# Kernel optimization log

Measured on AMD Instinct MI355X. Metric: run time of the kernel, lower is better.

Reference implementation:

```python
import jax, jax.numpy as jnp
import numpy as np

B = 64        # graphs per batch
N = 2048      # nodes per graph
BN = B * N
BE = BN * 16  # edges (avg degree 16)
C1 = 64
C2 = 64
M = 16
K_EDGES = 4   # hardcoded k=4 in original forward


def setup_inputs() -> dict:
    key = jax.random.key(0)
    k1, k2, k3, k4, k5, k6 = jax.random.split(key, 6)
    x = jax.random.normal(k1, (BN, C1), dtype=jnp.float32)
    e_ = jax.random.randint(k2, (2, BE), 0, BN, dtype=jnp.int32)
    b_ = jnp.repeat(jnp.arange(B, dtype=jnp.int32), N)  # sorted batch index
    # Linear params (stored as (in, out); torch stores (out, in))
    W_assign = jax.random.normal(k3, (C1, M), dtype=jnp.float32) / np.sqrt(C1)
    b_assign = jax.random.normal(k4, (M,), dtype=jnp.float32) * 0.01
    W_embed = jax.random.normal(k5, (C1, C2 - 3), dtype=jnp.float32) / np.sqrt(C1)
    b_embed = jax.random.normal(k6, (C2 - 3,), dtype=jnp.float32) * 0.01
    return {"x": x, "e_": e_, "b_": b_, "W_assign": W_assign,
            "b_assign": b_assign, "W_embed": W_embed, "b_embed": b_embed}


def reference(x, e_, b_, W_assign, b_assign, W_embed, b_embed):
    BN_, _ = x.shape
    Bn = int(jnp.max(b_)) + 1
    Mm = W_assign.shape[1]

    p = x[:, :3]                                   # (BN, 3) positions
    f = x @ W_embed + b_embed                      # (BN, C2-3)
    S = jax.nn.softmax(x @ W_assign + b_assign, axis=-1)  # (BN, M)

    # Weighted scatter-reduce pooling: index_add over (batch*M + m)
    # == per-batch segment_sum of S[n,m] * feat[n,c]
    Zf = jax.ops.segment_sum(S[:, :, None] * f[:, None, :], b_, num_segments=Bn)  # (B, M, C2-3)
    Zp = jax.ops.segment_sum(S[:, :, None] * p[:, None, :], b_, num_segments=Bn)  # (B, M, 3)
    w = jax.ops.segment_sum(S, b_, num_segments=Bn)                               # (B, M)
    w = jnp.maximum(w, 1e-10)
    Zp = Zp / w[..., None]
    x_out = jnp.concatenate([Zp, Zf], axis=-1).reshape(Bn * Mm, -1)  # (B*M, C2)

    # Sparse adjacency pooling: AS = A_NN @ S (A_NN[src,dst]=1 per edge)
    AS = jax.ops.segment_sum(S[e_[1]], e_[0], num_segments=BN_)  # (BN, M)
    # A_MM[b] = (S^T masked to batch b) @ AS
    A_MM = jax.ops.segment_sum(S[:, :, None] * AS[:, None, :], b_, num_segments=Bn)  # (B, M, M)

    # top-k edge construction on pooled adjacency
    dst = jax.lax.top_k(A_MM, K_EDGES)[1]                                # (B, M, k)
    src = jnp.broadcast_to(jnp.arange(Mm)[None, :, None], (Bn, Mm, K_EDGES))
    offset = (jnp.arange(Bn) * Mm)[:, None, None]
    e_out = jnp.stack([(src + offset).reshape(-1), (dst + offset).reshape(-1)], axis=0)
    b_out = jnp.repeat(jnp.arange(Bn), Mm)
    return x_out, e_out, b_out
```

## Files before the change

### kernel.cpp

```cpp
#include <hip/hip_runtime.h>

#define BN 131072
#define BE 2097152
#define NGR 64
#define CAP 36864

#define XS_OFF     0
#define WACC_OFF   262144
#define A_OFF      266240
#define ZERO_U4    20736
#define CUR_OFF    331776
#define QS_OFF     332032
#define ENDS_OFF   333056
#define SH_OFF     2430208
#define PK_OFF     6624512

__device__ __forceinline__ float bflo(unsigned u) { return __uint_as_float(u << 16); }
__device__ __forceinline__ float bfhi(unsigned u) { return __uint_as_float(u & 0xFFFF0000u); }

__global__ __launch_bounds__(256) void k_zero(uint4* __restrict__ zbase,
                                              int* __restrict__ cur)
{
    int zi = blockIdx.x * 256 + threadIdx.x;
    if (zi < ZERO_U4) zbase[zi] = make_uint4(0u, 0u, 0u, 0u);
    if (blockIdx.x == 0 && threadIdx.x < NGR) cur[threadIdx.x] = threadIdx.x * CAP;
}

__global__ __launch_bounds__(256) void k_scatter(const int* __restrict__ e_,
                                                 int* __restrict__ cur,
                                                 unsigned* __restrict__ packed)
{
    __shared__ int h[64];
    __shared__ int gb[64];
    int t = threadIdx.x;
    if (t < 64) h[t] = 0;
    __syncthreads();
    size_t base = (size_t)blockIdx.x * 4096;
    int e0v[16], e1v[16], rk[16];
    #pragma unroll
    for (int k = 0; k < 16; ++k) {
        size_t i = base + k * 256 + t;
        e0v[k] = e_[i];
        e1v[k] = e_[BE + i];
        rk[k] = atomicAdd(&h[e0v[k] >> 11], 1);
    }
    __syncthreads();
    if (t < 64) gb[t] = atomicAdd(&cur[t], h[t]);
    __syncthreads();
    #pragma unroll
    for (int k = 0; k < 16; ++k) {
        int b = e0v[k] >> 11;
        packed[gb[b] + rk[k]] = ((unsigned)(e0v[k] & 2047) << 17) | (unsigned)e1v[k];
    }
}

__global__ __launch_bounds__(256) void k_node(const float* __restrict__ x,
                                              const float* __restrict__ Wa,
                                              const float* __restrict__ ba,
                                              unsigned short* __restrict__ Sh,
                                              float* __restrict__ Xs,
                                              float* __restrict__ wacc)
{
    __shared__ __align__(16) float Xl[128 * 65];
    __shared__ __align__(16) float Sl[128 * 20];
    __shared__ float Wl[64 * 16];

    const int t = threadIdx.x;
    const int blk = blockIdx.x;
    const int g = blk >> 4;
    const int nd = t & 127;
    const int ch = t >> 7;

    const float4* xg4 = (const float4*)(x + (size_t)blk * 128 * 64);
    #pragma unroll
    for (int it = 0; it < 8; ++it) {
        int idx4 = it * 256 + t;
        float4 v = xg4[idx4];
        int node = idx4 >> 4;
        int c4 = (idx4 & 15) * 4;
        float* p = &Xl[node * 65 + c4];
        p[0] = v.x; p[1] = v.y; p[2] = v.z; p[3] = v.w;
    }
    for (int i = t; i < 1024; i += 256) Wl[i] = Wa[i];
    __syncthreads();

    float lg[16];
    #pragma unroll
    for (int m = 0; m < 16; ++m) lg[m] = 0.f;
    const int c0 = ch * 32;
    for (int c = c0; c < c0 + 32; ++c) {
        float xc = Xl[nd * 65 + c];
        #pragma unroll
        for (int m = 0; m < 16; ++m) lg[m] += xc * Wl[c * 16 + m];
    }
    float* Pl = Sl;
    if (ch == 1) {
        #pragma unroll
        for (int m = 0; m < 16; ++m) Pl[nd * 17 + m] = lg[m];
    }
    __syncthreads();

    float s[16];
    if (ch == 0) {
        float sum = 0.f, mx;
        #pragma unroll
        for (int m = 0; m < 16; ++m) lg[m] += ba[m] + Pl[nd * 17 + m];
        mx = lg[0];
        #pragma unroll
        for (int m = 1; m < 16; ++m) mx = fmaxf(mx, lg[m]);
        #pragma unroll
        for (int m = 0; m < 16; ++m) { s[m] = expf(lg[m] - mx); sum += s[m]; }
        float inv = 1.f / sum;
        #pragma unroll
        for (int m = 0; m < 16; ++m) s[m] *= inv;

        unsigned pk8[8];
        #pragma unroll
        for (int j = 0; j < 8; ++j) {
            unsigned b0 = __float_as_uint(s[2*j]);
            unsigned b1 = __float_as_uint(s[2*j+1]);
            unsigned h0 = (b0 + 0x7FFFu + ((b0 >> 16) & 1u)) >> 16;
            unsigned h1 = (b1 + 0x7FFFu + ((b1 >> 16) & 1u)) >> 16;
            pk8[j] = h0 | (h1 << 16);
        }
        uint4* hrow = (uint4*)(Sh + ((size_t)blk * 128 + nd) * 16);
        hrow[0] = make_uint4(pk8[0], pk8[1], pk8[2], pk8[3]);
        hrow[1] = make_uint4(pk8[4], pk8[5], pk8[6], pk8[7]);
    }
    __syncthreads();
    if (ch == 0) {
        #pragma unroll
        for (int q = 0; q < 4; ++q)
            *(float4*)(&Sl[nd * 20 + q * 4]) = make_float4(s[q*4], s[q*4+1], s[q*4+2], s[q*4+3]);
    }
    __syncthreads();

    const int c = t & 63;
    const int mg = t >> 6;
    float a0 = 0.f, a1 = 0.f, a2 = 0.f, a3 = 0.f;
    for (int n = 0; n < 128; ++n) {
        float xv = Xl[n * 65 + c];
        float4 sa = *(const float4*)(&Sl[n * 20 + mg * 4]);
        a0 += sa.x * xv; a1 += sa.y * xv; a2 += sa.z * xv; a3 += sa.w * xv;
    }
    float* xsg = Xs + g * 1024 + (mg * 4) * 64 + c;
    atomicAdd(&xsg[0],   a0);
    atomicAdd(&xsg[64],  a1);
    atomicAdd(&xsg[128], a2);
    atomicAdd(&xsg[192], a3);

    if (t < 16) {
        float ws_ = 0.f;
        for (int n = 0; n < 128; ++n) ws_ += Sl[n * 20 + t];
        atomicAdd(&wacc[g * 16 + t], ws_);
    }
}

#define SBUF_CAP 9216
__global__ __launch_bounds__(512) void k_sortL(unsigned* __restrict__ packed,
                                               const int* __restrict__ cur,
                                               int* __restrict__ qs,
                                               int* __restrict__ ends4)
{
    __shared__ unsigned sbuf[SBUF_CAP];
    __shared__ unsigned sout[SBUF_CAP];
    __shared__ int h[2048];
    __shared__ int psum[512];
    const int t = threadIdx.x;
    const int Q = blockIdx.x;
    const int g = Q >> 2;
    const int q = Q & 3;
    const int slab = g * CAP;
    const int n = cur[g] - slab;
    const int chunk = (n + 3) >> 2;
    const int qlo = slab + min(q * chunk, n);
    const int qhi = slab + min((q + 1) * chunk, n);
    const int nq = qhi - qlo;
    if (t == 0) qs[Q] = qlo;

    for (int i = t; i < 2048; i += 512) h[i] = 0;
    __syncthreads();
    for (int i = t; i < nq; i += 512) {
        unsigned u = packed[qlo + i];
        sbuf[i] = u;
        atomicAdd(&h[u >> 17], 1);
    }
    __syncthreads();

    int hl[4]; int s = 0;
    #pragma unroll
    for (int j = 0; j < 4; ++j) { hl[j] = h[t * 4 + j]; s += hl[j]; }
    psum[t] = s;
    __syncthreads();
    for (int off = 1; off < 512; off <<= 1) {
        int v = (t >= off) ? psum[t - off] : 0;
        __syncthreads();
        psum[t] += v;
        __syncthreads();
    }
    int run = psum[t] - s;
    int* ends = ends4 + (Q << 11);
    #pragma unroll
    for (int j = 0; j < 4; ++j) {
        int bin = t * 4 + j;
        int c = hl[j];
        h[bin] = run;
        run += c;
        ends[bin] = qlo + run;
    }
    __syncthreads();
    for (int i = t; i < nq; i += 512) {
        unsigned u = sbuf[i];
        int pos = atomicAdd(&h[u >> 17], 1);
        sout[pos] = u & 131071u;
    }
    __syncthreads();
    for (int i = t; i < nq; i += 512) packed[qlo + i] = sout[i];
}

__global__ __launch_bounds__(256) void k_edge(const unsigned* __restrict__ se1,
                                              const unsigned short* __restrict__ Sh,
                                              const int* __restrict__ ends4,
                                              const int* __restrict__ qs,
                                              float* __restrict__ A)
{
    __shared__ __align__(16) float ASl[64 * 16];
    const int t = threadIdx.x;
    const int blk = blockIdx.x;
    const int g = blk >> 5;
    const int nbase = blk << 6;

    {
        const int qd = t >> 2;
        const int c4 = (t & 3) << 2;
        const int nl = (nbase & 2047) + qd;
        const unsigned short* __restrict__ ShB = Sh + c4;

        int lo[4], hi[4];
        #pragma unroll
        for (int q = 0; q < 4; ++q) {
            const int Qb = (g << 2) + q;
            const int* __restrict__ ends = ends4 + (Qb << 11);
            lo[q] = nl ? ends[nl - 1] : qs[Qb];
            hi[q] = ends[nl];
        }

        float a0 = 0.f, a1 = 0.f, a2 = 0.f, a3 = 0.f;
        #pragma unroll
        for (int q = 0; q < 4; ++q) {
            int i = lo[q];
            const int h2 = hi[q];
            for (; i + 4 <= h2; i += 4) {
                unsigned ea = se1[i];
                unsigned eb = se1[i + 1];
                unsigned ec = se1[i + 2];
                unsigned ed = se1[i + 3];
                uint2 ra = *(const uint2*)(ShB + ((size_t)ea << 4));
                uint2 rb = *(const uint2*)(ShB + ((size_t)eb << 4));
                uint2 rc = *(const uint2*)(ShB + ((size_t)ec << 4));
                uint2 rd = *(const uint2*)(ShB + ((size_t)ed << 4));
                a0 += bflo(ra.x) + bflo(rb.x) + bflo(rc.x) + bflo(rd.x);
                a1 += bfhi(ra.x) + bfhi(rb.x) + bfhi(rc.x) + bfhi(rd.x);
                a2 += bflo(ra.y) + bflo(rb.y) + bflo(rc.y) + bflo(rd.y);
                a3 += bfhi(ra.y) + bfhi(rb.y) + bfhi(rc.y) + bfhi(rd.y);
            }
            for (; i < h2; ++i) {
                unsigned ea = se1[i];
                uint2 ra = *(const uint2*)(ShB + ((size_t)ea << 4));
                a0 += bflo(ra.x); a1 += bfhi(ra.x); a2 += bflo(ra.y); a3 += bfhi(ra.y);
            }
        }
        *(float4*)(&ASl[qd * 16 + c4]) = make_float4(a0, a1, a2, a3);
    }
    __syncthreads();

    {
        const int m = t >> 4;
        const int k = t & 15;
        const unsigned short* __restrict__ SgM = Sh + ((size_t)nbase << 4) + m;
        float a = 0.f;
        #pragma unroll 4
        for (int i = 0; i < 64; ++i) {
            float sv = __uint_as_float((unsigned)SgM[(size_t)i << 4] << 16);
            a += sv * ASl[i * 16 + k];
        }
        atomicAdd(&A[(g << 8) + t], a);
    }
}

__global__ __launch_bounds__(256) void k_xt(const float* __restrict__ Xs,
                                            const float* __restrict__ wacc,
                                            const float* __restrict__ We,
                                            const float* __restrict__ be,
                                            const float* __restrict__ A,
                                            float* __restrict__ out)
{
    const int t = threadIdx.x;
    const int blk = blockIdx.x;
    if (blk < 256) {
        int lane = t & 63;
        int row = blk * 4 + (t >> 6);
        const float* xs = Xs + row * 64;
        float w = wacc[row];
        float val;
        if (lane < 3) {
            val = xs[lane] / fmaxf(w, 1e-10f);
        } else {
            int c2 = lane - 3;
            float accv = w * be[c2];
            for (int cc = 0; cc < 64; ++cc) accv += xs[cc] * We[cc * 61 + c2];
            val = accv;
        }
        out[row * 64 + lane] = val;
    } else {
        int r = (blk - 256) * 256 + t;
        float v[16];
        #pragma unroll
        for (int i = 0; i < 16; ++i) v[i] = A[r * 16 + i];
        float* e0o = out + 65536;
        float* e1o = out + 65536 + 4096;
        float* bo  = out + 65536 + 8192;
        unsigned mask = 0;
        #pragma unroll
        for (int rep = 0; rep < 4; ++rep) {
            float best = -3.4e38f; int bi = 0;
            #pragma unroll
            for (int i = 0; i < 16; ++i) {
                bool ok = (((mask >> i) & 1u) == 0u) && (v[i] > best);
                if (ok) { best = v[i]; bi = i; }
            }
            mask |= (1u << bi);
            e0o[r * 4 + rep] = (float)r;
            e1o[r * 4 + rep] = (float)((r & ~15) + bi);
        }
        bo[r] = (float)(r >> 4);
    }
}

extern "C" void kernel_launch(void* const* d_in, const int* in_sizes, int n_in,
                              void* d_out, int out_size, void* d_ws, size_t ws_size,
                              hipStream_t stream)
{
    const float* x  = (const float*)d_in[0];
    const int*   e  = (const int*)d_in[1];
    const float* Wa = (const float*)d_in[3];
    const float* ba = (const float*)d_in[4];
    const float* We = (const float*)d_in[5];
    const float* be = (const float*)d_in[6];

    char* ws = (char*)d_ws;
    float* Xs     = (float*)(ws + XS_OFF);
    float* wacc   = (float*)(ws + WACC_OFF);
    float* A      = (float*)(ws + A_OFF);
    int*   cur    = (int*)(ws + CUR_OFF);
    int*   qs     = (int*)(ws + QS_OFF);
    int*   ends4  = (int*)(ws + ENDS_OFF);
    unsigned short* Sh = (unsigned short*)(ws + SH_OFF);
    unsigned* packed = (unsigned*)(ws + PK_OFF);

    k_zero    <<<82, 256, 0, stream>>>((uint4*)ws, cur);
    k_scatter <<<512, 256, 0, stream>>>(e, cur, packed);
    k_node    <<<1024, 256, 0, stream>>>(x, Wa, ba, Sh, Xs, wacc);
    k_sortL   <<<256, 512, 0, stream>>>(packed, cur, qs, ends4);
    k_edge    <<<2048, 256, 0, stream>>>(packed, Sh, ends4, qs, A);
    k_xt      <<<260, 256, 0, stream>>>(Xs, wacc, We, be, A, (float*)d_out);
}
```

Measured before the change: 93.77 us.

## Fuse node projection and per-graph edge sort into one launch

Merges the softmax/pooling node kernel and the local edge sort into a single heterogeneous launch. The first 256 blocks do the sort and the rest do node work, so the two independent stages overlap and one launch is dropped. The sort now uses 256 threads, re-reads packed from global instead of buffering it in shared memory, and shares a union shared buffer with the node path. That union raises per-block LDS for the node path. Also switches expf to __expf and stages W_embed in shared memory in the final kernel, which every block now loads, including the top-k blocks.

```diff
diff --git a/kernel.cpp b/kernel.cpp
--- a/kernel.cpp
+++ b/kernel.cpp
@@ -54,24 +54,84 @@
     }
 }
 
-__global__ __launch_bounds__(256) void k_node(const float* __restrict__ x,
-                                              const float* __restrict__ Wa,
-                                              const float* __restrict__ ba,
-                                              unsigned short* __restrict__ Sh,
-                                              float* __restrict__ Xs,
-                                              float* __restrict__ wacc)
-{
-    __shared__ __align__(16) float Xl[128 * 65];
-    __shared__ __align__(16) float Sl[128 * 20];
-    __shared__ float Wl[64 * 16];
-
+__global__ __launch_bounds__(256) void k_nodeSort(const float* __restrict__ x,
+                                                  const float* __restrict__ Wa,
+                                                  const float* __restrict__ ba,
+                                                  unsigned short* __restrict__ Sh,
+                                                  float* __restrict__ Xs,
+                                                  float* __restrict__ wacc,
+                                                  unsigned* __restrict__ packed,
+                                                  const int* __restrict__ cur,
+                                                  int* __restrict__ qs,
+                                                  int* __restrict__ ends4)
+{
+    __shared__ __align__(16) unsigned char smem[47616];
     const int t = threadIdx.x;
     const int blk = blockIdx.x;
-    const int g = blk >> 4;
+
+    if (blk < 256) {
+        unsigned* sout = (unsigned*)smem;
+        int* h    = (int*)(smem + 36864);
+        int* psum = (int*)(smem + 45056);
+        const int Q = blk;
+        const int g = Q >> 2;
+        const int q = Q & 3;
+        const int slab = g * CAP;
+        const int n = cur[g] - slab;
+        const int chunk = (n + 3) >> 2;
+        const int qlo = slab + min(q * chunk, n);
+        const int qhi = slab + min((q + 1) * chunk, n);
+        const int nq = qhi - qlo;
+        if (t == 0) qs[Q] = qlo;
+
+        for (int i = t; i < 2048; i += 256) h[i] = 0;
+        __syncthreads();
+        for (int i = t; i < nq; i += 256) {
+            atomicAdd(&h[packed[qlo + i] >> 17], 1);
+        }
+        __syncthreads();
+
+        int hl[8]; int s = 0;
+        #pragma unroll
+        for (int j = 0; j < 8; ++j) { hl[j] = h[t * 8 + j]; s += hl[j]; }
+        psum[t] = s;
+        __syncthreads();
+        for (int off = 1; off < 256; off <<= 1) {
+            int v = (t >= off) ? psum[t - off] : 0;
+            __syncthreads();
+            psum[t] += v;
+            __syncthreads();
+        }
+        int run = psum[t] - s;
+        int* ends = ends4 + (Q << 11);
+        #pragma unroll
+        for (int j = 0; j < 8; ++j) {
+            int bin = t * 8 + j;
+            int c = hl[j];
+            h[bin] = run;
+            run += c;
+            ends[bin] = qlo + run;
+        }
+        __syncthreads();
+        for (int i = t; i < nq; i += 256) {
+            unsigned u = packed[qlo + i];
+            int pos = atomicAdd(&h[u >> 17], 1);
+            sout[pos] = u & 131071u;
+        }
+        __syncthreads();
+        for (int i = t; i < nq; i += 256) packed[qlo + i] = sout[i];
+        return;
+    }
+
+    const int nblk = blk - 256;
+    const int g = nblk >> 4;
+    float* Xl = (float*)smem;
+    float* Sl = (float*)(smem + 33280);
+    float* Wl = (float*)(smem + 43520);
     const int nd = t & 127;
     const int ch = t >> 7;
 
-    const float4* xg4 = (const float4*)(x + (size_t)blk * 128 * 64);
+    const float4* xg4 = (const float4*)(x + (size_t)nblk * 128 * 64);
     #pragma unroll
     for (int it = 0; it < 8; ++it) {
         int idx4 = it * 256 + t;
@@ -109,7 +169,7 @@
         #pragma unroll
         for (int m = 1; m < 16; ++m) mx = fmaxf(mx, lg[m]);
         #pragma unroll
-        for (int m = 0; m < 16; ++m) { s[m] = expf(lg[m] - mx); sum += s[m]; }
+        for (int m = 0; m < 16; ++m) { s[m] = __expf(lg[m] - mx); sum += s[m]; }
         float inv = 1.f / sum;
         #pragma unroll
         for (int m = 0; m < 16; ++m) s[m] *= inv;
@@ -123,7 +183,7 @@
             unsigned h1 = (b1 + 0x7FFFu + ((b1 >> 16) & 1u)) >> 16;
             pk8[j] = h0 | (h1 << 16);
         }
-        uint4* hrow = (uint4*)(Sh + ((size_t)blk * 128 + nd) * 16);
+        uint4* hrow = (uint4*)(Sh + ((size_t)nblk * 128 + nd) * 16);
         hrow[0] = make_uint4(pk8[0], pk8[1], pk8[2], pk8[3]);
         hrow[1] = make_uint4(pk8[4], pk8[5], pk8[6], pk8[7]);
     }
@@ -154,68 +214,6 @@
         for (int n = 0; n < 128; ++n) ws_ += Sl[n * 20 + t];
         atomicAdd(&wacc[g * 16 + t], ws_);
     }
-}
-
-#define SBUF_CAP 9216
-__global__ __launch_bounds__(512) void k_sortL(unsigned* __restrict__ packed,
-                                               const int* __restrict__ cur,
-                                               int* __restrict__ qs,
-                                               int* __restrict__ ends4)
-{
-    __shared__ unsigned sbuf[SBUF_CAP];
-    __shared__ unsigned sout[SBUF_CAP];
-    __shared__ int h[2048];
-    __shared__ int psum[512];
-    const int t = threadIdx.x;
-    const int Q = blockIdx.x;
-    const int g = Q >> 2;
-    const int q = Q & 3;
-    const int slab = g * CAP;
-    const int n = cur[g] - slab;
-    const int chunk = (n + 3) >> 2;
-    const int qlo = slab + min(q * chunk, n);
-    const int qhi = slab + min((q + 1) * chunk, n);
-    const int nq = qhi - qlo;
-    if (t == 0) qs[Q] = qlo;
-
-    for (int i = t; i < 2048; i += 512) h[i] = 0;
-    __syncthreads();
-    for (int i = t; i < nq; i += 512) {
-        unsigned u = packed[qlo + i];
-        sbuf[i] = u;
-        atomicAdd(&h[u >> 17], 1);
-    }
-    __syncthreads();
-
-    int hl[4]; int s = 0;
-    #pragma unroll
-    for (int j = 0; j < 4; ++j) { hl[j] = h[t * 4 + j]; s += hl[j]; }
-    psum[t] = s;
-    __syncthreads();
-    for (int off = 1; off < 512; off <<= 1) {
-        int v = (t >= off) ? psum[t - off] : 0;
-        __syncthreads();
-        psum[t] += v;
-        __syncthreads();
-    }
-    int run = psum[t] - s;
-    int* ends = ends4 + (Q << 11);
-    #pragma unroll
-    for (int j = 0; j < 4; ++j) {
-        int bin = t * 4 + j;
-        int c = hl[j];
-        h[bin] = run;
-        run += c;
-        ends[bin] = qlo + run;
-    }
-    __syncthreads();
-    for (int i = t; i < nq; i += 512) {
-        unsigned u = sbuf[i];
-        int pos = atomicAdd(&h[u >> 17], 1);
-        sout[pos] = u & 131071u;
-    }
-    __syncthreads();
-    for (int i = t; i < nq; i += 512) packed[qlo + i] = sout[i];
 }
 
 __global__ __launch_bounds__(256) void k_edge(const unsigned* __restrict__ se1,
@@ -295,8 +293,12 @@
                                             const float* __restrict__ A,
                                             float* __restrict__ out)
 {
+    __shared__ float WeL[64 * 61];
     const int t = threadIdx.x;
     const int blk = blockIdx.x;
+    for (int i = t; i < 64 * 61; i += 256) WeL[i] = We[i];
+    __syncthreads();
+
     if (blk < 256) {
         int lane = t & 63;
         int row = blk * 4 + (t >> 6);
@@ -308,7 +310,7 @@
         } else {
             int c2 = lane - 3;
             float accv = w * be[c2];
-            for (int cc = 0; cc < 64; ++cc) accv += xs[cc] * We[cc * 61 + c2];
+            for (int cc = 0; cc < 64; ++cc) accv += xs[cc] * WeL[cc * 61 + c2];
             val = accv;
         }
         out[row * 64 + lane] = val;
@@ -360,8 +362,7 @@
 
     k_zero    <<<82, 256, 0, stream>>>((uint4*)ws, cur);
     k_scatter <<<512, 256, 0, stream>>>(e, cur, packed);
-    k_node    <<<1024, 256, 0, stream>>>(x, Wa, ba, Sh, Xs, wacc);
-    k_sortL   <<<256, 512, 0, stream>>>(packed, cur, qs, ends4);
+    k_nodeSort<<<1280, 256, 0, stream>>>(x, Wa, ba, Sh, Xs, wacc, packed, cur, qs, ends4);
     k_edge    <<<2048, 256, 0, stream>>>(packed, Sh, ends4, qs, A);
     k_xt      <<<260, 256, 0, stream>>>(Xs, wacc, We, be, A, (float*)d_out);
 }
```

After: 87.87 us. -6.3%, faster.

## Merge scatter with node kernel and x-transform with edge kernel

Applied to the files above, without the earlier changes.

Combines the edge scatter and node softmax/pooling kernels into one launch split by block index, and likewise runs the pooled-feature embedding blocks inside the edge adjacency kernel, leaving top-k as a small separate launch. The aim is to cut launch gaps and let independent work overlap on the GPU. It also stages W_embed in shared memory and switches to fast __expf. The cost is a larger shared-memory footprint per block for the scatter path, which may lower its occupancy, plus slightly less accurate softmax.

```diff
diff --git a/kernel.cpp b/kernel.cpp
--- a/kernel.cpp
+++ b/kernel.cpp
@@ -17,6 +17,13 @@
 
 __device__ __forceinline__ float bflo(unsigned u) { return __uint_as_float(u << 16); }
 __device__ __forceinline__ float bfhi(unsigned u) { return __uint_as_float(u & 0xFFFF0000u); }
+__device__ __forceinline__ unsigned bfpack(float a, float b) {
+    unsigned b0 = __float_as_uint(a);
+    unsigned b1 = __float_as_uint(b);
+    unsigned h0 = (b0 + 0x7FFFu + ((b0 >> 16) & 1u)) >> 16;
+    unsigned h1 = (b1 + 0x7FFFu + ((b1 >> 16) & 1u)) >> 16;
+    return h0 | (h1 << 16);
+}
 
 __global__ __launch_bounds__(256) void k_zero(uint4* __restrict__ zbase,
                                               int* __restrict__ cur)
@@ -26,52 +33,54 @@
     if (blockIdx.x == 0 && threadIdx.x < NGR) cur[threadIdx.x] = threadIdx.x * CAP;
 }
 
-__global__ __launch_bounds__(256) void k_scatter(const int* __restrict__ e_,
-                                                 int* __restrict__ cur,
-                                                 unsigned* __restrict__ packed)
-{
-    __shared__ int h[64];
-    __shared__ int gb[64];
-    int t = threadIdx.x;
-    if (t < 64) h[t] = 0;
-    __syncthreads();
-    size_t base = (size_t)blockIdx.x * 4096;
-    int e0v[16], e1v[16], rk[16];
-    #pragma unroll
-    for (int k = 0; k < 16; ++k) {
-        size_t i = base + k * 256 + t;
-        e0v[k] = e_[i];
-        e1v[k] = e_[BE + i];
-        rk[k] = atomicAdd(&h[e0v[k] >> 11], 1);
-    }
-    __syncthreads();
-    if (t < 64) gb[t] = atomicAdd(&cur[t], h[t]);
-    __syncthreads();
-    #pragma unroll
-    for (int k = 0; k < 16; ++k) {
-        int b = e0v[k] >> 11;
-        packed[gb[b] + rk[k]] = ((unsigned)(e0v[k] & 2047) << 17) | (unsigned)e1v[k];
-    }
-}
-
-__global__ __launch_bounds__(256) void k_node(const float* __restrict__ x,
-                                              const float* __restrict__ Wa,
-                                              const float* __restrict__ ba,
-                                              unsigned short* __restrict__ Sh,
-                                              float* __restrict__ Xs,
-                                              float* __restrict__ wacc)
-{
-    __shared__ __align__(16) float Xl[128 * 65];
-    __shared__ __align__(16) float Sl[128 * 20];
-    __shared__ float Wl[64 * 16];
-
+__global__ __launch_bounds__(256) void k_scatNode2(const int* __restrict__ e_,
+                                                   int* __restrict__ cur,
+                                                   unsigned* __restrict__ packed,
+                                                   const float* __restrict__ x,
+                                                   const float* __restrict__ Wa,
+                                                   const float* __restrict__ ba,
+                                                   unsigned short* __restrict__ Sh,
+                                                   float* __restrict__ Xs,
+                                                   float* __restrict__ wacc)
+{
+    __shared__ __align__(16) unsigned char smem[47616];
     const int t = threadIdx.x;
     const int blk = blockIdx.x;
-    const int g = blk >> 4;
+
+    if (blk < 512) {
+        int* h  = (int*)smem;
+        int* gb = (int*)(smem + 256);
+        if (t < 64) h[t] = 0;
+        __syncthreads();
+        size_t base = (size_t)blk * 4096;
+        int e0v[16], e1v[16], rk[16];
+        #pragma unroll
+        for (int k = 0; k < 16; ++k) {
+            size_t i = base + k * 256 + t;
+            e0v[k] = e_[i];
+            e1v[k] = e_[BE + i];
+            rk[k] = atomicAdd(&h[e0v[k] >> 11], 1);
+        }
+        __syncthreads();
+        if (t < 64) gb[t] = atomicAdd(&cur[t], h[t]);
+        __syncthreads();
+        #pragma unroll
+        for (int k = 0; k < 16; ++k) {
+            int b = e0v[k] >> 11;
+            packed[gb[b] + rk[k]] = ((unsigned)(e0v[k] & 2047) << 17) | (unsigned)e1v[k];
+        }
+        return;
+    }
+
+    const int nblk = blk - 512;
+    const int g = nblk >> 4;
+    float* Xl = (float*)smem;
+    float* Sl = (float*)(smem + 33280);
+    float* Wl = (float*)(smem + 43520);
     const int nd = t & 127;
     const int ch = t >> 7;
 
-    const float4* xg4 = (const float4*)(x + (size_t)blk * 128 * 64);
+    const float4* xg4 = (const float4*)(x + (size_t)nblk * 128 * 64);
     #pragma unroll
     for (int it = 0; it < 8; ++it) {
         int idx4 = it * 256 + t;
@@ -109,21 +118,15 @@
         #pragma unroll
         for (int m = 1; m < 16; ++m) mx = fmaxf(mx, lg[m]);
         #pragma unroll
-        for (int m = 0; m < 16; ++m) { s[m] = expf(lg[m] - mx); sum += s[m]; }
+        for (int m = 0; m < 16; ++m) { s[m] = __expf(lg[m] - mx); sum += s[m]; }
         float inv = 1.f / sum;
         #pragma unroll
         for (int m = 0; m < 16; ++m) s[m] *= inv;
 
         unsigned pk8[8];
         #pragma unroll
-        for (int j = 0; j < 8; ++j) {
-            unsigned b0 = __float_as_uint(s[2*j]);
-            unsigned b1 = __float_as_uint(s[2*j+1]);
-            unsigned h0 = (b0 + 0x7FFFu + ((b0 >> 16) & 1u)) >> 16;
-            unsigned h1 = (b1 + 0x7FFFu + ((b1 >> 16) & 1u)) >> 16;
-            pk8[j] = h0 | (h1 << 16);
-        }
-        uint4* hrow = (uint4*)(Sh + ((size_t)blk * 128 + nd) * 16);
+        for (int j = 0; j < 8; ++j) pk8[j] = bfpack(s[2*j], s[2*j+1]);
+        uint4* hrow = (uint4*)(Sh + ((size_t)nblk * 128 + nd) * 16);
         hrow[0] = make_uint4(pk8[0], pk8[1], pk8[2], pk8[3]);
         hrow[1] = make_uint4(pk8[4], pk8[5], pk8[6], pk8[7]);
     }
@@ -218,17 +221,46 @@
     for (int i = t; i < nq; i += 512) packed[qlo + i] = sout[i];
 }
 
-__global__ __launch_bounds__(256) void k_edge(const unsigned* __restrict__ se1,
-                                              const unsigned short* __restrict__ Sh,
-                                              const int* __restrict__ ends4,
-                                              const int* __restrict__ qs,
-                                              float* __restrict__ A)
-{
-    __shared__ __align__(16) float ASl[64 * 16];
+__global__ __launch_bounds__(256) void k_edgeX(const unsigned* __restrict__ se1,
+                                               const unsigned short* __restrict__ Sh,
+                                               const int* __restrict__ ends4,
+                                               const int* __restrict__ qs,
+                                               float* __restrict__ A,
+                                               const float* __restrict__ Xs,
+                                               const float* __restrict__ wacc,
+                                               const float* __restrict__ We,
+                                               const float* __restrict__ be,
+                                               float* __restrict__ out)
+{
+    __shared__ __align__(16) unsigned char smem[15616];
     const int t = threadIdx.x;
     const int blk = blockIdx.x;
-    const int g = blk >> 5;
-    const int nbase = blk << 6;
+
+    if (blk < 256) {
+        float* WeL = (float*)smem;
+        for (int i = t; i < 64 * 61; i += 256) WeL[i] = We[i];
+        __syncthreads();
+        int lane = t & 63;
+        int row = blk * 4 + (t >> 6);
+        const float* xs = Xs + row * 64;
+        float w = wacc[row];
+        float val;
+        if (lane < 3) {
+            val = xs[lane] / fmaxf(w, 1e-10f);
+        } else {
+            int c2 = lane - 3;
+            float accv = w * be[c2];
+            for (int cc = 0; cc < 64; ++cc) accv += xs[cc] * WeL[cc * 61 + c2];
+            val = accv;
+        }
+        out[row * 64 + lane] = val;
+        return;
+    }
+
+    float* ASl = (float*)smem;
+    const int eblk = blk - 256;
+    const int g = eblk >> 5;
+    const int nbase = eblk << 6;
 
     {
         const int qd = t >> 2;
@@ -288,53 +320,30 @@
     }
 }
 
-__global__ __launch_bounds__(256) void k_xt(const float* __restrict__ Xs,
-                                            const float* __restrict__ wacc,
-                                            const float* __restrict__ We,
-                                            const float* __restrict__ be,
-                                            const float* __restrict__ A,
-                                            float* __restrict__ out)
-{
-    const int t = threadIdx.x;
-    const int blk = blockIdx.x;
-    if (blk < 256) {
-        int lane = t & 63;
-        int row = blk * 4 + (t >> 6);
-        const float* xs = Xs + row * 64;
-        float w = wacc[row];
-        float val;
-        if (lane < 3) {
-            val = xs[lane] / fmaxf(w, 1e-10f);
-        } else {
-            int c2 = lane - 3;
-            float accv = w * be[c2];
-            for (int cc = 0; cc < 64; ++cc) accv += xs[cc] * We[cc * 61 + c2];
-            val = accv;
-        }
-        out[row * 64 + lane] = val;
-    } else {
-        int r = (blk - 256) * 256 + t;
-        float v[16];
-        #pragma unroll
-        for (int i = 0; i < 16; ++i) v[i] = A[r * 16 + i];
-        float* e0o = out + 65536;
-        float* e1o = out + 65536 + 4096;
-        float* bo  = out + 65536 + 8192;
-        unsigned mask = 0;
-        #pragma unroll
-        for (int rep = 0; rep < 4; ++rep) {
-            float best = -3.4e38f; int bi = 0;
-            #pragma unroll
-            for (int i = 0; i < 16; ++i) {
-                bool ok = (((mask >> i) & 1u) == 0u) && (v[i] > best);
-                if (ok) { best = v[i]; bi = i; }
-            }
-            mask |= (1u << bi);
-            e0o[r * 4 + rep] = (float)r;
-            e1o[r * 4 + rep] = (float)((r & ~15) + bi);
-        }
-        bo[r] = (float)(r >> 4);
-    }
+__global__ __launch_bounds__(256) void k_topk(const float* __restrict__ A,
+                                              float* __restrict__ out)
+{
+    int r = blockIdx.x * 256 + threadIdx.x;
+    float v[16];
+    #pragma unroll
+    for (int i = 0; i < 16; ++i) v[i] = A[r * 16 + i];
+    float* e0o = out + 65536;
+    float* e1o = out + 65536 + 4096;
+    float* bo  = out + 65536 + 8192;
+    unsigned mask = 0;
+    #pragma unroll
+    for (int rep = 0; rep < 4; ++rep) {
+        float best = -3.4e38f; int bi = 0;
+        #pragma unroll
+        for (int i = 0; i < 16; ++i) {
+            bool ok = (((mask >> i) & 1u) == 0u) && (v[i] > best);
+            if (ok) { best = v[i]; bi = i; }
+        }
+        mask |= (1u << bi);
+        e0o[r * 4 + rep] = (float)r;
+        e1o[r * 4 + rep] = (float)((r & ~15) + bi);
+    }
+    bo[r] = (float)(r >> 4);
 }
 
 extern "C" void kernel_launch(void* const* d_in, const int* in_sizes, int n_in,
@@ -358,10 +367,9 @@
     unsigned short* Sh = (unsigned short*)(ws + SH_OFF);
     unsigned* packed = (unsigned*)(ws + PK_OFF);
 
-    k_zero    <<<82, 256, 0, stream>>>((uint4*)ws, cur);
-    k_scatter <<<512, 256, 0, stream>>>(e, cur, packed);
-    k_node    <<<1024, 256, 0, stream>>>(x, Wa, ba, Sh, Xs, wacc);
-    k_sortL   <<<256, 512, 0, stream>>>(packed, cur, qs, ends4);
-    k_edge    <<<2048, 256, 0, stream>>>(packed, Sh, ends4, qs, A);
-    k_xt      <<<260, 256, 0, stream>>>(Xs, wacc, We, be, A, (float*)d_out);
-}
+    k_zero     <<<82, 256, 0, stream>>>((uint4*)ws, cur);
+    k_scatNode2<<<1536, 256, 0, stream>>>(e, cur, packed, x, Wa, ba, Sh, Xs, wacc);
+    k_sortL    <<<256, 512, 0, stream>>>(packed, cur, qs, ends4);
+    k_edgeX    <<<2304, 256, 0, stream>>>(packed, Sh, ends4, qs, A, Xs, wacc, We, be, (float*)d_out);
+    k_topk     <<<4, 256, 0, stream>>>(A, (float*)d_out);
+}
```

New measurement: 96.24 us. 2.6% more time.
